# Optimization experiments

Hardware: AMD Instinct MI355X
Metric: run time of the kernel (lower is better)

## Reference

```python
import jax, jax.numpy as jnp
import numpy as np

N = 500_000   # num nodes
F = 128       # num_features
H = 128       # hidden
B = 32_768    # batch size
K = 4         # hops
RWS = 16      # random walks per batch node
E = RWS * B   # sampled edges per hop
ALPHA = 0.1
OUT = 8


def setup_inputs() -> dict:
    key = jax.random.key(0)
    ks = jax.random.split(key, 12)
    x = jax.random.normal(ks[0], (N, F), dtype=jnp.float32)
    degree = jax.random.uniform(ks[1], (N,), dtype=jnp.float32, minval=1.0, maxval=64.0)
    batch = jax.random.randint(ks[2], (B,), 0, N, dtype=jnp.int32)
    heads_idx = jax.random.randint(ks[3], (K, E), 0, B, dtype=jnp.int32)
    ends = jax.random.randint(ks[4], (K, E), 0, N, dtype=jnp.int32)
    # MLP params (Kaiming-ish scaling)
    W0 = jax.random.normal(ks[5], (F, H), dtype=jnp.float32) / np.float32(np.sqrt(F))
    b0 = jnp.zeros((H,), dtype=jnp.float32)
    W1 = jax.random.normal(ks[6], (H, H), dtype=jnp.float32) / np.float32(np.sqrt(H))
    b1 = jnp.zeros((H,), dtype=jnp.float32)
    W2 = jax.random.normal(ks[7], (H, OUT), dtype=jnp.float32) / np.float32(np.sqrt(H))
    b2 = jnp.zeros((OUT,), dtype=jnp.float32)
    # APPNP attention weights: alpha*(1-alpha)^k, last = (1-alpha)^K
    att = np.float32(ALPHA) * np.float32(1.0 - ALPHA) ** np.arange(K + 1, dtype=np.float32)
    att[-1] = np.float32(1.0 - ALPHA) ** np.float32(K)
    att = jnp.asarray(att)
    return {"x": x, "W0": W0, "b0": b0, "W1": W1, "b1": b1, "W2": W2, "b2": b2,
            "att": att, "degree": degree, "batch": batch,
            "heads_idx": heads_idx, "ends": ends}


def reference(x, W0, b0, W1, b1, W2, b2, att, degree, batch, heads_idx, ends):
    # eval mode: dropout is a no-op
    dis = degree ** -0.5  # deg_inv_sqrt

    def mlp(feats):  # lins[1](relu(lins[0](feats)))
        h = jax.nn.relu(feats @ W0 + b0)
        return h @ W1 + b1

    nb = batch.shape[0]
    ne = jnp.float32(ends.shape[1])
    dsum = degree[batch].sum()

    aggx = att[0] * mlp(x[batch])                       # [B, H]
    for k in range(K):  # small fixed hop count
        heads = heads_idx[k]                            # local rows in [0, B)
        e = ends[k]                                     # global node ids
        val = dis[batch[heads]] * dis[e] * (dsum / ne)  # [E]
        tmp = mlp(x[e]) * val[:, None]                  # gather + MLP + weight
        aggx = aggx + att[k + 1] * jax.ops.segment_sum(tmp, heads, num_segments=nb)
    out = jax.nn.relu(aggx) @ W2 + b2                   # [B, 8]
    return jax.nn.log_softmax(out, axis=1)
```

## Files before the change

### kernel.cpp

```cpp
#include <hip/hip_runtime.h>

#define NN 500000
#define FF 128
#define HH 128
#define BB 32768
#define KHOPS 4
#define EPER 524288
#define KE (KHOPS * EPER)
#define NOUT 8
#define SBLK 256
#define EPB (KE / SBLK)
#define GEMM_TILES 3907

typedef unsigned short u16;
typedef unsigned char u8;
typedef __attribute__((ext_vector_type(8))) short short8v;
typedef __attribute__((ext_vector_type(4))) float f32x4;

__device__ __forceinline__ float bflo(unsigned int u) {
    union { unsigned int x; float f; } t; t.x = u << 16; return t.f;
}
__device__ __forceinline__ float bfhi(unsigned int u) {
    union { unsigned int x; float f; } t; t.x = u & 0xFFFF0000u; return t.f;
}
__device__ __forceinline__ u16 f2bf(float f) {
    union { float f; unsigned int u; } t; t.f = f;
    unsigned int u = t.u;
    unsigned int r = (u + 0x7FFFu + ((u >> 16) & 1u)) >> 16;
    return (u16)r;
}

__global__ void k_degsum1(const float* __restrict__ deg, const int* __restrict__ batch,
                          float* __restrict__ partial) {
    __shared__ float red[256];
    int i = blockIdx.x * 256 + threadIdx.x;
    red[threadIdx.x] = deg[batch[i]];
    __syncthreads();
    for (int off = 128; off > 0; off >>= 1) {
        if (threadIdx.x < off) red[threadIdx.x] += red[threadIdx.x + off];
        __syncthreads();
    }
    if (threadIdx.x == 0) partial[blockIdx.x] = red[0];
}
__global__ void k_degsum2(const float* __restrict__ partial, float* __restrict__ dsum) {
    __shared__ float red[128];
    red[threadIdx.x] = partial[threadIdx.x];
    __syncthreads();
    for (int off = 64; off > 0; off >>= 1) {
        if (threadIdx.x < off) red[threadIdx.x] += red[threadIdx.x + off];
        __syncthreads();
    }
    if (threadIdx.x == 0) *dsum = red[0];
}

__global__ void k_prep(const float* __restrict__ deg, const int* __restrict__ batch,
                       const float* __restrict__ dsum,
                       float* __restrict__ dis, float* __restrict__ disb) {
    int i = blockIdx.x * 256 + threadIdx.x;
    if (i < NN) dis[i] = rsqrtf(deg[i]);
    if (i < BB) disb[i] = rsqrtf(deg[batch[i]]) * (dsum[0] * (1.0f / (float)EPER));
}

__launch_bounds__(256, 2)
__global__ void k_hist2(const int* __restrict__ heads, u8* __restrict__ M) {
    __shared__ unsigned int hp[8192];
    int tid = threadIdx.x, blk = blockIdx.x;
    #pragma unroll
    for (int j = 0; j < 32; j++) hp[tid + j * 256] = 0;
    __syncthreads();
    int ebase = blk * EPB;
    #pragma unroll 4
    for (int it = 0; it < EPB / 256; it++) {
        int b = heads[ebase + it * 256 + tid];
        atomicAdd(&hp[b >> 2], 1u << ((b & 3) * 8));
    }
    __syncthreads();
    unsigned int* M32 = (unsigned int*)(M + (size_t)blk * BB);
    #pragma unroll
    for (int j = 0; j < 32; j++) {
        int w = tid + j * 256;
        M32[w] = hp[w];
    }
}

__global__ void k_colscan(u8* __restrict__ M, int* __restrict__ colsum) {
    int key = blockIdx.x * 256 + threadIdx.x;
    unsigned int run = 0;
    #pragma unroll 8
    for (int b = 0; b < SBLK; b++) {
        size_t idx = (size_t)b * BB + key;
        u8 v = M[idx];
        M[idx] = (u8)run;
        run += v;
    }
    colsum[key] = (int)run;
}

__global__ void k_scan(const int* __restrict__ colsum, int* __restrict__ base) {
    __shared__ int sc[1024];
    int tid = threadIdx.x;
    int loc[32];
    int run = 0;
    #pragma unroll
    for (int j = 0; j < 32; j++) {
        loc[j] = run;
        run += colsum[tid * 32 + j];
    }
    sc[tid] = run;
    __syncthreads();
    for (int off = 1; off < 1024; off <<= 1) {
        int v = (tid >= off) ? sc[tid - off] : 0;
        __syncthreads();
        sc[tid] += v;
        __syncthreads();
    }
    int excl = sc[tid] - run;
    #pragma unroll
    for (int j = 0; j < 32; j++) base[tid * 32 + j] = excl + loc[j];
    if (tid == 1023) base[BB] = sc[1023];
}

__global__ void k_packW0(const float* __restrict__ W0, u16* __restrict__ w0p) {
    int f = blockIdx.x * 256 + threadIdx.x;
    int k = f >> 7, c = f & 127;
    int kt = k >> 5, i = k & 7, lh = (k >> 3) & 3;
    int lane = lh * 16 + (c & 15), n = c >> 4;
    w0p[(((kt * 8 + n) * 64 + lane) << 3) + i] = f2bf(W0[f]);
}

__launch_bounds__(256, 2)
__global__ void k_fused(const float* __restrict__ x, const u16* __restrict__ w0p,
                        const float* __restrict__ b0, u16* __restrict__ h,
                        const int* __restrict__ heads, const int* __restrict__ ends,
                        const u8* __restrict__ M, const int* __restrict__ base,
                        unsigned int* __restrict__ pe) {
    __shared__ u16 ws[16384];
    int tid = threadIdx.x;

    if (blockIdx.x < SBLK) {
        unsigned int* hp = (unsigned int*)ws;
        int blk = blockIdx.x;
        #pragma unroll
        for (int j = 0; j < 32; j++) hp[tid + j * 256] = 0;
        __syncthreads();
        int ebase = blk * EPB;
        for (int it = 0; it < EPB / 256; it++) {
            int i = ebase + it * 256 + tid;
            int b = heads[i];
            unsigned int e = (unsigned int)ends[i];
            unsigned int kk = (unsigned int)(i >> 19);
            unsigned int old = atomicAdd(&hp[b >> 2], 1u << ((b & 3) * 8));
            unsigned int rank = (old >> ((b & 3) * 8)) & 0xFFu;
            int pos = base[b] + (int)M[(size_t)blk * BB + b] + (int)rank;
            pe[pos] = (kk << 19) | e;
        }
        return;
    }

    int wid = tid >> 6;
    int lane = tid & 63;
    long rowbase = (long)(blockIdx.x - SBLK) * 128;

    #pragma unroll
    for (int r = 0; r < 8; r++) {
        int f = tid + r * 256;
        *(float4*)&ws[f * 8] = *(const float4*)&w0p[f * 8];
    }

    short8v a[2][4];
    int qc = (lane >> 4) * 8;
    #pragma unroll
    for (int rs = 0; rs < 2; rs++) {
        long grow = rowbase + wid * 32 + rs * 16 + (lane & 15);
        if (grow >= NN) grow = NN - 1;
        const float* xr = &x[grow * 128 + qc];
        #pragma unroll
        for (int kt = 0; kt < 4; kt++) {
            float4 v0 = *(const float4*)&xr[kt * 32];
            float4 v1 = *(const float4*)&xr[kt * 32 + 4];
            short8v f;
            f[0] = (short)f2bf(v0.x); f[1] = (short)f2bf(v0.y);
            f[2] = (short)f2bf(v0.z); f[3] = (short)f2bf(v0.w);
            f[4] = (short)f2bf(v1.x); f[5] = (short)f2bf(v1.y);
            f[6] = (short)f2bf(v1.z); f[7] = (short)f2bf(v1.w);
            a[rs][kt] = f;
        }
    }
    __syncthreads();

    f32x4 acc[2][8] = {};
    #pragma unroll
    for (int n = 0; n < 8; n++) {
        short8v bfr[4];
        #pragma unroll
        for (int kt = 0; kt < 4; kt++)
            bfr[kt] = *(const short8v*)&ws[(((kt * 8 + n) * 64 + lane) << 3)];
        #pragma unroll
        for (int rs = 0; rs < 2; rs++) {
            #pragma unroll
            for (int kt = 0; kt < 4; kt++)
                acc[rs][n] = __builtin_amdgcn_mfma_f32_16x16x32_bf16(
                                 a[rs][kt], bfr[kt], acc[rs][n], 0, 0, 0);
        }
    }

    float b0v[8];
    #pragma unroll
    for (int n = 0; n < 8; n++) b0v[n] = b0[n * 16 + (lane & 15)];

    __syncthreads();
    u16* xw = &ws[wid * 32 * 128];
    #pragma unroll
    for (int rs = 0; rs < 2; rs++) {
        #pragma unroll
        for (int r = 0; r < 4; r++) {
            int row = rs * 16 + (lane >> 4) * 4 + r;
            int sw = (row & 7) << 4;
            #pragma unroll
            for (int n = 0; n < 8; n++) {
                float v = acc[rs][n][r] + b0v[n];
                v = v > 0.f ? v : 0.f;
                int byte = row * 256 + ((n * 32 + (lane & 15) * 2) ^ sw);
                *(u16*)((char*)xw + byte) = f2bf(v);
            }
        }
    }
    __syncthreads();
    #pragma unroll
    for (int pass = 0; pass < 8; pass++) {
        int off = pass * 1024 + lane * 16;
        int row = off >> 8;
        int colb = off & 255;
        int ocolb = colb ^ ((row & 7) << 4);
        long grow = rowbase + wid * 32 + row;
        uint4 v = *(const uint4*)((const char*)xw + off);
        if (grow < NN)
            *(uint4*)((char*)&h[grow * 128] + ocolb) = v;
    }
}

__launch_bounds__(256)
__global__ void k_gather(const u16* __restrict__ h, const int* __restrict__ batch,
                         const int* __restrict__ base, const unsigned int* __restrict__ pe,
                         const float* __restrict__ dis, const float* __restrict__ disb,
                         const float* __restrict__ att,
                         float* __restrict__ P, float* __restrict__ s) {
    int b = blockIdx.x * 4 + (threadIdx.x >> 6);
    int l = threadIdx.x & 63;
    int q = l >> 4;
    int c8 = (l & 15) * 8;
    float att0 = att[0];
    float a1 = att[1], a2 = att[2], a3 = att[3], a4 = att[4];
    float dbv = disb[b];
    float acc[8] = {0.f, 0.f, 0.f, 0.f, 0.f, 0.f, 0.f, 0.f};

    if (q == 0) {
        int nb = batch[b];
        uint4 v = *(const uint4*)&h[(size_t)nb * 128 + c8];
        acc[0] = att0 * bflo(v.x); acc[1] = att0 * bfhi(v.x);
        acc[2] = att0 * bflo(v.y); acc[3] = att0 * bfhi(v.y);
        acc[4] = att0 * bflo(v.z); acc[5] = att0 * bfhi(v.z);
        acc[6] = att0 * bflo(v.w); acc[7] = att0 * bfhi(v.w);
    }

    int beg = base[b], fin = base[b + 1];
    float wsum = 0.f;
    for (int j = beg; j < fin; j += 32) {
        unsigned int p[8];
        #pragma unroll
        for (int u = 0; u < 8; u++) {
            int je = j + u * 4 + q;
            int jc = je < fin ? je : beg;
            p[u] = pe[jc];
            if (je >= fin) p[u] |= 0x80000000u;
        }
        float wv[8];
        uint4 v[8];
        #pragma unroll
        for (int u = 0; u < 8; u++) {
            int e = (int)(p[u] & 0x7FFFFu);
            int kk = (int)((p[u] >> 19) & 3u);
            float av = (kk < 2) ? (kk == 0 ? a1 : a2) : (kk == 2 ? a3 : a4);
            float w = av * dbv * dis[e];
            wv[u] = (p[u] & 0x80000000u) ? 0.f : w;
            v[u] = *(const uint4*)&h[(size_t)e * 128 + c8];
        }
        #pragma unroll
        for (int u = 0; u < 8; u++) {
            float w = wv[u];
            acc[0] += w * bflo(v[u].x); acc[1] += w * bfhi(v[u].x);
            acc[2] += w * bflo(v[u].y); acc[3] += w * bfhi(v[u].y);
            acc[4] += w * bflo(v[u].z); acc[5] += w * bfhi(v[u].z);
            acc[6] += w * bflo(v[u].w); acc[7] += w * bfhi(v[u].w);
            wsum += w;
        }
    }
    #pragma unroll
    for (int k = 0; k < 8; k++) {
        acc[k] += __shfl_xor(acc[k], 16);
        acc[k] += __shfl_xor(acc[k], 32);
    }
    wsum += __shfl_xor(wsum, 16);
    wsum += __shfl_xor(wsum, 32);

    if (q == 0) {
        float4 o0 = { acc[0], acc[1], acc[2], acc[3] };
        float4 o1 = { acc[4], acc[5], acc[6], acc[7] };
        *(float4*)&P[(size_t)b * 128 + c8]     = o0;
        *(float4*)&P[(size_t)b * 128 + c8 + 4] = o1;
        if (l == 0) s[b] = att0 + wsum;
    }
}

__launch_bounds__(256, 2)
__global__ void k_out(const float* __restrict__ P, const float* __restrict__ s,
                      const float* __restrict__ W1, const float* __restrict__ b1,
                      const float* __restrict__ W2, const float* __restrict__ b2,
                      float* __restrict__ out) {
    __shared__ float W1s[128 * 128];
    __shared__ float Ps[32 * 128];
    int tid = threadIdx.x;
    int rowbase = blockIdx.x * 32;
    #pragma unroll
    for (int rep = 0; rep < 16; rep++) {
        int f = tid + rep * 256;
        *(float4*)&W1s[f * 4] = *(const float4*)&W1[f * 4];
    }
    #pragma unroll
    for (int rep = 0; rep < 4; rep++) {
        int f = tid + rep * 256;
        *(float4*)&Ps[f * 4] = *(const float4*)&P[(size_t)rowbase * 128 + f * 4];
    }
    __syncthreads();

    int c0 = (tid & 31) * 4;
    int r0 = (tid >> 5) * 4;
    float b1r[4] = { b1[c0], b1[c0 + 1], b1[c0 + 2], b1[c0 + 3] };
    float sv[4];
    #pragma unroll
    for (int j = 0; j < 4; j++) sv[j] = s[rowbase + r0 + j];

    float acc[4][4] = {};
    #pragma unroll 2
    for (int i = 0; i < 128; i += 4) {
        float4 xq[4], wq4[4];
        #pragma unroll
        for (int j = 0; j < 4; j++) xq[j]  = *(const float4*)&Ps[(r0 + j) * 128 + i];
        #pragma unroll
        for (int q = 0; q < 4; q++) wq4[q] = *(const float4*)&W1s[(i + q) * 128 + c0];
        #pragma unroll
        for (int j = 0; j < 4; j++) {
            float xv[4] = { xq[j].x, xq[j].y, xq[j].z, xq[j].w };
            #pragma unroll
            for (int q = 0; q < 4; q++) {
                acc[j][0] += xv[q] * wq4[q].x;
                acc[j][1] += xv[q] * wq4[q].y;
                acc[j][2] += xv[q] * wq4[q].z;
                acc[j][3] += xv[q] * wq4[q].w;
            }
        }
    }
    __syncthreads();
    #pragma unroll
    for (int j = 0; j < 4; j++) {
        #pragma unroll
        for (int c = 0; c < 4; c++) {
            float v = acc[j][c] + sv[j] * b1r[c];
            Ps[(r0 + j) * 128 + c0 + c] = v > 0.f ? v : 0.f;
        }
    }
    __syncthreads();

    int row = tid >> 3;
    int o = tid & 7;
    int rot = (row * 4) & 127;
    float v = b2[o];
    #pragma unroll 4
    for (int ii = 0; ii < 128; ii++) {
        int i = (ii + rot) & 127;
        v += Ps[row * 128 + i] * W2[i * 8 + o];
    }
    float m = v;
    for (int d = 1; d < 8; d <<= 1) m = fmaxf(m, __shfl_xor(m, d, 8));
    float ex = expf(v - m);
    float sum = ex;
    for (int d = 1; d < 8; d <<= 1) sum += __shfl_xor(sum, d, 8);
    out[(size_t)(rowbase + row) * 8 + o] = (v - m) - logf(sum);
}

extern "C" void kernel_launch(void* const* d_in, const int* in_sizes, int n_in,
                              void* d_out, int out_size, void* d_ws, size_t ws_size,
                              hipStream_t stream) {
    const float* x     = (const float*)d_in[0];
    const float* W0    = (const float*)d_in[1];
    const float* b0    = (const float*)d_in[2];
    const float* W1    = (const float*)d_in[3];
    const float* b1    = (const float*)d_in[4];
    const float* W2    = (const float*)d_in[5];
    const float* b2    = (const float*)d_in[6];
    const float* att   = (const float*)d_in[7];
    const float* deg   = (const float*)d_in[8];
    const int*   batch = (const int*)d_in[9];
    const int*   heads = (const int*)d_in[10];
    const int*   ends  = (const int*)d_in[11];
    float* out = (float*)d_out;

    char* w = (char*)d_ws;
    size_t off = 0;
    u16* h = (u16*)(w + off);          off += (size_t)NN * 128 * 2;
    float* P = (float*)(w + off);      off += (size_t)BB * 128 * 4;
    float* s = (float*)(w + off);      off += (size_t)BB * 4;
    int* base = (int*)(w + off);       off += 131328;
    unsigned int* pe = (unsigned int*)(w + off); off += (size_t)KE * 4;
    u8* M = (u8*)(w + off);            off += (size_t)SBLK * BB;
    int* colsum = (int*)(w + off);     off += (size_t)BB * 4;
    float* dis = (float*)(w + off);    off += (size_t)NN * 4;
    float* disb = (float*)(w + off);   off += (size_t)BB * 4;
    float* partial = (float*)(w + off); off += 1024;
    float* dsum = (float*)(w + off);   off += 256;
    u16* w0p = (u16*)(w + off);        off += 16384 * 2;

    k_degsum1<<<128, 256, 0, stream>>>(deg, batch, partial);
    k_degsum2<<<1, 128, 0, stream>>>(partial, dsum);
    k_prep<<<(NN + 255) / 256, 256, 0, stream>>>(deg, batch, dsum, dis, disb);
    k_hist2<<<SBLK, 256, 0, stream>>>(heads, M);
    k_colscan<<<BB / 256, 256, 0, stream>>>(M, colsum);
    k_scan<<<1, 1024, 0, stream>>>(colsum, base);
    k_packW0<<<64, 256, 0, stream>>>(W0, w0p);
    k_fused<<<SBLK + GEMM_TILES, 256, 0, stream>>>(x, w0p, b0, h, heads, ends,
                                                   M, base, pe);
    k_gather<<<BB / 4, 256, 0, stream>>>(h, batch, base, pe, dis, disb, att, P, s);
    k_out<<<BB / 32, 256, 0, stream>>>(P, s, W1, b1, W2, b2, out);
}
```

Baseline: 312.2 us.

## Stage x and W0 tiles into LDS via direct global-to-LDS loads with smaller tiles

The fused GEMM blocks now load the bf16 W0 pack and a 64-row fp32 x tile straight into LDS using global_load_lds, with an XOR swizzle on the x rows. Each wave then reads its A fragments from LDS instead of issuing strided global loads into registers. The tile drops from 128 to 64 rows per block, which doubles the GEMM grid and halves per-wave accumulators, raising occupancy and latency hiding. In exchange it adds 32KB of LDS per block and repeats the W0 load in twice as many blocks.

```diff
diff --git a/kernel.cpp b/kernel.cpp
--- a/kernel.cpp
+++ b/kernel.cpp
@@ -10,7 +10,7 @@
 #define NOUT 8
 #define SBLK 256
 #define EPB (KE / SBLK)
-#define GEMM_TILES 3907
+#define GEMM_TILES 7813
 
 typedef unsigned short u16;
 typedef unsigned char u8;
@@ -28,6 +28,11 @@
     unsigned int u = t.u;
     unsigned int r = (u + 0x7FFFu + ((u >> 16) & 1u)) >> 16;
     return (u16)r;
+}
+__device__ __forceinline__ void gload_lds16(const void* g, void* l) {
+    __builtin_amdgcn_global_load_lds(
+        (const __attribute__((address_space(1))) void*)g,
+        (__attribute__((address_space(3))) void*)l, 16, 0, 0);
 }
 
 __global__ void k_degsum1(const float* __restrict__ deg, const int* __restrict__ batch,
@@ -134,6 +139,7 @@
                         const int* __restrict__ heads, const int* __restrict__ ends,
                         const u8* __restrict__ M, const int* __restrict__ base,
                         unsigned int* __restrict__ pe) {
+    __shared__ float xs[8192];
     __shared__ u16 ws[16384];
     int tid = threadIdx.x;
 
@@ -159,36 +165,46 @@
 
     int wid = tid >> 6;
     int lane = tid & 63;
-    long rowbase = (long)(blockIdx.x - SBLK) * 128;
-
-    #pragma unroll
-    for (int r = 0; r < 8; r++) {
-        int f = tid + r * 256;
-        *(float4*)&ws[f * 8] = *(const float4*)&w0p[f * 8];
-    }
-
-    short8v a[2][4];
-    int qc = (lane >> 4) * 8;
-    #pragma unroll
-    for (int rs = 0; rs < 2; rs++) {
-        long grow = rowbase + wid * 32 + rs * 16 + (lane & 15);
-        if (grow >= NN) grow = NN - 1;
-        const float* xr = &x[grow * 128 + qc];
+    long rowbase = (long)(blockIdx.x - SBLK) * 64;
+
+    #pragma unroll
+    for (int it = 0; it < 8; it++) {
+        int cbase = it * 256 + wid * 64;
+        gload_lds16((const char*)w0p + (size_t)(cbase + lane) * 16,
+                    (char*)ws + (size_t)cbase * 16);
+    }
+    #pragma unroll
+    for (int it = 0; it < 8; it++) {
+        int cbase = it * 256 + wid * 64;
+        int ci = cbase + lane;
+        int row = ci >> 5;
+        int p = ci & 31;
+        int c = p ^ (row & 7);
+        long grow = rowbase + row; if (grow >= NN) grow = NN - 1;
+        gload_lds16((const char*)x + (grow << 9) + (c << 4),
+                    (char*)xs + (size_t)cbase * 16);
+    }
+    __syncthreads();
+
+    short8v a[4];
+    {
+        int r = wid * 16 + (lane & 15);
+        int sw = r & 7;
         #pragma unroll
         for (int kt = 0; kt < 4; kt++) {
-            float4 v0 = *(const float4*)&xr[kt * 32];
-            float4 v1 = *(const float4*)&xr[kt * 32 + 4];
+            int c0 = kt * 8 + (lane >> 4) * 2;
+            float4 v0 = *(const float4*)((const char*)xs + r * 512 + ((c0 ^ sw) << 4));
+            float4 v1 = *(const float4*)((const char*)xs + r * 512 + (((c0 + 1) ^ sw) << 4));
             short8v f;
             f[0] = (short)f2bf(v0.x); f[1] = (short)f2bf(v0.y);
             f[2] = (short)f2bf(v0.z); f[3] = (short)f2bf(v0.w);
             f[4] = (short)f2bf(v1.x); f[5] = (short)f2bf(v1.y);
             f[6] = (short)f2bf(v1.z); f[7] = (short)f2bf(v1.w);
-            a[rs][kt] = f;
-        }
-    }
-    __syncthreads();
-
-    f32x4 acc[2][8] = {};
+            a[kt] = f;
+        }
+    }
+
+    f32x4 acc[8] = {};
     #pragma unroll
     for (int n = 0; n < 8; n++) {
         short8v bfr[4];
@@ -196,12 +212,9 @@
         for (int kt = 0; kt < 4; kt++)
             bfr[kt] = *(const short8v*)&ws[(((kt * 8 + n) * 64 + lane) << 3)];
         #pragma unroll
-        for (int rs = 0; rs < 2; rs++) {
-            #pragma unroll
-            for (int kt = 0; kt < 4; kt++)
-                acc[rs][n] = __builtin_amdgcn_mfma_f32_16x16x32_bf16(
-                                 a[rs][kt], bfr[kt], acc[rs][n], 0, 0, 0);
-        }
+        for (int kt = 0; kt < 4; kt++)
+            acc[n] = __builtin_amdgcn_mfma_f32_16x16x32_bf16(a[kt], bfr[kt],
+                                                             acc[n], 0, 0, 0);
     }
 
     float b0v[8];
@@ -209,30 +222,27 @@
     for (int n = 0; n < 8; n++) b0v[n] = b0[n * 16 + (lane & 15)];
 
     __syncthreads();
-    u16* xw = &ws[wid * 32 * 128];
-    #pragma unroll
-    for (int rs = 0; rs < 2; rs++) {
-        #pragma unroll
-        for (int r = 0; r < 4; r++) {
-            int row = rs * 16 + (lane >> 4) * 4 + r;
-            int sw = (row & 7) << 4;
-            #pragma unroll
-            for (int n = 0; n < 8; n++) {
-                float v = acc[rs][n][r] + b0v[n];
-                v = v > 0.f ? v : 0.f;
-                int byte = row * 256 + ((n * 32 + (lane & 15) * 2) ^ sw);
-                *(u16*)((char*)xw + byte) = f2bf(v);
-            }
-        }
-    }
-    __syncthreads();
-    #pragma unroll
-    for (int pass = 0; pass < 8; pass++) {
+    u16* xw = (u16*)xs + wid * 16 * 128;
+    #pragma unroll
+    for (int r = 0; r < 4; r++) {
+        int row = (lane >> 4) * 4 + r;
+        int sw = (row & 7) << 4;
+        #pragma unroll
+        for (int n = 0; n < 8; n++) {
+            float v = acc[n][r] + b0v[n];
+            v = v > 0.f ? v : 0.f;
+            int byte = row * 256 + ((n * 32 + (lane & 15) * 2) ^ sw);
+            *(u16*)((char*)xw + byte) = f2bf(v);
+        }
+    }
+    __syncthreads();
+    #pragma unroll
+    for (int pass = 0; pass < 4; pass++) {
         int off = pass * 1024 + lane * 16;
         int row = off >> 8;
         int colb = off & 255;
         int ocolb = colb ^ ((row & 7) << 4);
-        long grow = rowbase + wid * 32 + row;
+        long grow = rowbase + wid * 16 + row;
         uint4 v = *(const uint4*)((const char*)xw + off);
         if (grow < NN)
             *(uint4*)((char*)&h[grow * 128] + ocolb) = v;
```

Result: no change. 317.6 us (+1.7%).
